# Performance work log

Hardware: AMD Instinct MI355X
Metric: run time of the kernel (lower is better)

## Reference

```python
import jax, jax.numpy as jnp
import numpy as np

HIDDEN = 4096   # hidden_dim
RANK = 16       # lora_rank
ALPHA = 32.0    # lora_alpha
BATCH = 4
SEQ = 4096
TWO_OVER_PI = 2.0 / np.pi


def setup_inputs() -> dict:
    key = jax.random.key(0)
    kx, ka, kb, ksa, ksb = jax.random.split(key, 5)
    x = jax.random.normal(kx, (BATCH, SEQ, HIDDEN), dtype=jnp.float32)
    # int8 pi/2 coefficients (stored as int8, symmetric range)
    A_int8 = jax.random.randint(ka, (HIDDEN, RANK), -127, 128, dtype=jnp.int32).astype(jnp.int8)
    B_int8 = jax.random.randint(kb, (RANK, HIDDEN), -127, 128, dtype=jnp.int32).astype(jnp.int8)
    # per-column (output-channel) dequant scales, small positive values
    scale_A = jax.random.uniform(ksa, (RANK,), jnp.float32, 1e-3, 1e-2)
    scale_B = jax.random.uniform(ksb, (HIDDEN,), jnp.float32, 1e-3, 1e-2)
    return {"x": x, "A_int8": A_int8, "B_int8": B_int8,
            "scale_A": scale_A, "scale_B": scale_B}


def reference(x, A_int8, B_int8, scale_A, scale_B):
    # Dequantize: per-column scale (scale has shape [cols])
    A = A_int8.astype(jnp.float32) * scale_A[None, :]   # [H, R]
    B = B_int8.astype(jnp.float32) * scale_B[None, :]   # [R, H]
    # Low-rank path: x @ A @ B  (rank-16 bottleneck kept explicit)
    h = jnp.einsum('bsh,hr->bsr', x, A)                 # [B, S, R]
    h = jnp.einsum('bsr,rh->bsh', h, B)                 # [B, S, H]
    # y = x + (alpha/r) * sin(h * 2/pi)
    return x + (ALPHA / RANK) * jnp.sin(h * TWO_OVER_PI)
```

## Files before the change

kernel.cpp:

```cpp
#include <hip/hip_runtime.h>

#define H       4096
#define RANK    16
#define NROWS   16384
#define RPB     2
#define TPB     256
#define TWO_OVER_PI 0.63661977236758134f

typedef float f32x4 __attribute__((ext_vector_type(4)));

__global__ __launch_bounds__(256) void pack_ab(const int* __restrict__ A32,
                                               const int* __restrict__ B32,
                                               unsigned int* __restrict__ A8,
                                               unsigned int* __restrict__ B8) {
    int i = blockIdx.x * 256 + threadIdx.x;
    int4 a = ((const int4*)A32)[i];
    A8[i] = ((unsigned)((a.x + 128) & 0xff))       | ((unsigned)((a.y + 128) & 0xff) << 8) |
            ((unsigned)((a.z + 128) & 0xff) << 16) | ((unsigned)((a.w + 128) & 0xff) << 24);

    int c = i & 3, tt = (i >> 2) & 255, r = i >> 10;
    int4 b = ((const int4*)B32)[r * 1024 + c * 256 + tt];
    B8[i] = ((unsigned)((b.x + 128) & 0xff))       | ((unsigned)((b.y + 128) & 0xff) << 8) |
            ((unsigned)((b.z + 128) & 0xff) << 16) | ((unsigned)((b.w + 128) & 0xff) << 24);
}

__global__ __launch_bounds__(TPB, 4) void pilora_fused(
    const float* __restrict__ x,
    const unsigned int* __restrict__ A8,
    const unsigned int* __restrict__ B8,
    const float* __restrict__ sA,
    const float* __restrict__ sB,
    float* __restrict__ out)
{
    const int t    = threadIdx.x;
    const int lane = t & 63;
    const int wid  = t >> 6;
    const int row0 = blockIdx.x * RPB;

    __shared__ __attribute__((aligned(16))) float xs[RPB * H];
    __shared__ float wsum[4][32];
    __shared__ __attribute__((aligned(16))) float hsh[32];
    __shared__ float HsLds[RPB];

    const float* xrow = x + (size_t)row0 * H;
    #pragma unroll
    for (int i = 0; i < 8; ++i) {
        __builtin_amdgcn_global_load_lds(
            (const __attribute__((address_space(1))) unsigned int*)(xrow + i * 1024 + t * 4),
            (__attribute__((address_space(3)))       unsigned int*)(xs   + i * 1024 + t * 4),
            16, 0, 0);
    }
    __syncthreads();

    float w[32];
    #pragma unroll
    for (int j = 0; j < 32; ++j) w[j] = 0.0f;
    float sx0 = 0.0f, sx1 = 0.0f;

    const int4* A16 = (const int4*)A8;
    #pragma unroll
    for (int c = 0; c < 4; ++c) {
        f32x4 xv0 = *(const f32x4*)&xs[      c * 1024 + t * 4];
        f32x4 xv1 = *(const f32x4*)&xs[H +   c * 1024 + t * 4];
        #pragma unroll
        for (int e = 0; e < 4; ++e) {
            int4 q = A16[c * 1024 + t * 4 + e];
            float x0 = xv0[e], x1 = xv1[e];
            sx0 += x0; sx1 += x1;
            int qw[4] = {q.x, q.y, q.z, q.w};
            #pragma unroll
            for (int wi = 0; wi < 4; ++wi) {
                unsigned uw = (unsigned)qw[wi];
                #pragma unroll
                for (int b = 0; b < 4; ++b) {
                    float u = (float)((uw >> (8 * b)) & 0xffu);
                    w[     wi * 4 + b] += x0 * u;
                    w[16 + wi * 4 + b] += x1 * u;
                }
            }
        }
    }
    #pragma unroll
    for (int j = 0; j < 16; ++j) { w[j] -= 128.0f * sx0; w[16 + j] -= 128.0f * sx1; }

    #pragma unroll
    for (int b = 0; b < 5; ++b) {
        int q = (lane >> b) & 1;
        #pragma unroll
        for (int k = 0; k < (16 >> b); ++k) {
            float keep  = q ? w[2 * k + 1] : w[2 * k];
            float send  = q ? w[2 * k]     : w[2 * k + 1];
            float other = __shfl_xor(send, 1 << b, 64);
            w[k] = keep + other;
        }
    }
    w[0] += __shfl_xor(w[0], 32, 64);

    if (lane < 32) wsum[wid][lane] = w[0];
    __syncthreads();

    if (t < 32) {
        float v = wsum[0][t] + wsum[1][t] + wsum[2][t] + wsum[3][t];
        int r = t & 15, rr = t >> 4;
        float hv = v * sA[r];
        hsh[r * 2 + rr] = hv;
        float hs = hv;
        hs += __shfl_xor(hs, 1, 64);
        hs += __shfl_xor(hs, 2, 64);
        hs += __shfl_xor(hs, 4, 64);
        hs += __shfl_xor(hs, 8, 64);
        if (r == 0) HsLds[rr] = 128.0f * hs;
    }
    __syncthreads();

    float hf[32];
    #pragma unroll
    for (int k = 0; k < 8; ++k) *(f32x4*)&hf[k * 4] = *(const f32x4*)&hsh[k * 4];
    float hs0 = HsLds[0], hs1 = HsLds[1];

    float g0[16], g1[16];
    #pragma unroll
    for (int j = 0; j < 16; ++j) { g0[j] = -hs0; g1[j] = -hs1; }

    const int4* Bp = (const int4*)B8;
    #pragma unroll
    for (int r = 0; r < RANK; ++r) {
        float h0 = hf[r * 2 + 0], h1 = hf[r * 2 + 1];
        int4 bw = Bp[r * 256 + t];
        int bwa[4] = {bw.x, bw.y, bw.z, bw.w};
        #pragma unroll
        for (int wi = 0; wi < 4; ++wi) {
            unsigned uw = (unsigned)bwa[wi];
            #pragma unroll
            for (int b = 0; b < 4; ++b) {
                float u = (float)((uw >> (8 * b)) & 0xffu);
                g0[wi * 4 + b] += h0 * u;
                g1[wi * 4 + b] += h1 * u;
            }
        }
    }

    const float4* sB4 = (const float4*)sB;
    f32x4* o4 = (f32x4*)out;
    #pragma unroll
    for (int c = 0; c < 4; ++c) {
        float4 sb = sB4[c * 256 + t];
        float k0 = sb.x * TWO_OVER_PI;
        float k1 = sb.y * TWO_OVER_PI;
        float k2 = sb.z * TWO_OVER_PI;
        float k3 = sb.w * TWO_OVER_PI;
        f32x4 xv0 = *(const f32x4*)&xs[    c * 1024 + t * 4];
        f32x4 xv1 = *(const f32x4*)&xs[H + c * 1024 + t * 4];
        f32x4 o0, o1;
        o0[0] = xv0[0] + 2.0f * __sinf(g0[c * 4 + 0] * k0);
        o0[1] = xv0[1] + 2.0f * __sinf(g0[c * 4 + 1] * k1);
        o0[2] = xv0[2] + 2.0f * __sinf(g0[c * 4 + 2] * k2);
        o0[3] = xv0[3] + 2.0f * __sinf(g0[c * 4 + 3] * k3);
        o1[0] = xv1[0] + 2.0f * __sinf(g1[c * 4 + 0] * k0);
        o1[1] = xv1[1] + 2.0f * __sinf(g1[c * 4 + 1] * k1);
        o1[2] = xv1[2] + 2.0f * __sinf(g1[c * 4 + 2] * k2);
        o1[3] = xv1[3] + 2.0f * __sinf(g1[c * 4 + 3] * k3);
        __builtin_nontemporal_store(o0, &o4[(size_t)(row0 + 0) * 1024 + c * 256 + t]);
        __builtin_nontemporal_store(o1, &o4[(size_t)(row0 + 1) * 1024 + c * 256 + t]);
    }
}

extern "C" void kernel_launch(void* const* d_in, const int* in_sizes, int n_in,
                              void* d_out, int out_size, void* d_ws, size_t ws_size,
                              hipStream_t stream) {
    const float* x   = (const float*)d_in[0];
    const int*   A32 = (const int*)d_in[1];
    const int*   B32 = (const int*)d_in[2];
    const float* sA  = (const float*)d_in[3];
    const float* sB  = (const float*)d_in[4];
    float*       out = (float*)d_out;

    unsigned int* A8 = (unsigned int*)d_ws;
    unsigned int* B8 = A8 + (H * RANK / 4);

    pack_ab<<<(H * RANK / 4) / 256, 256, 0, stream>>>(A32, B32, A8, B8);
    pilora_fused<<<NROWS / RPB, TPB, 0, stream>>>(
        x, A8, B8, sA, sB, out);
}
```

Measured before the change: 465.8 us.

## Process four rows per block with packed FMA and drop LDS staging of x

Each block now handles four rows instead of two, so each int8 weight unpack serves four rows. Accumulation uses 2-wide float vectors so the compiler can emit packed FMA. The LDS staging of x through global_load_lds is removed: x is read straight from global memory in the reduction phase and read a second time in the output phase, counting on cache hits. The risks are a second read of x that may miss the caches and higher register pressure from 64 accumulators per thread.

```diff
diff --git a/kernel.cpp b/kernel.cpp
--- a/kernel.cpp
+++ b/kernel.cpp
@@ -3,11 +3,12 @@
 #define H       4096
 #define RANK    16
 #define NROWS   16384
-#define RPB     2
+#define RPB     4
 #define TPB     256
 #define TWO_OVER_PI 0.63661977236758134f
 
 typedef float f32x4 __attribute__((ext_vector_type(4)));
+typedef float f32x2 __attribute__((ext_vector_type(2)));
 
 __global__ __launch_bounds__(256) void pack_ab(const int* __restrict__ A32,
                                                const int* __restrict__ B32,
@@ -37,36 +38,30 @@
     const int wid  = t >> 6;
     const int row0 = blockIdx.x * RPB;
 
-    __shared__ __attribute__((aligned(16))) float xs[RPB * H];
-    __shared__ float wsum[4][32];
-    __shared__ __attribute__((aligned(16))) float hsh[32];
+    __shared__ float wsum[4][64];
+    __shared__ __attribute__((aligned(16))) float hsh[64];
     __shared__ float HsLds[RPB];
 
-    const float* xrow = x + (size_t)row0 * H;
+    const f32x4* x4 = (const f32x4*)x;
+
+    f32x2 w01[16], w23[16];
     #pragma unroll
-    for (int i = 0; i < 8; ++i) {
-        __builtin_amdgcn_global_load_lds(
-            (const __attribute__((address_space(1))) unsigned int*)(xrow + i * 1024 + t * 4),
-            (__attribute__((address_space(3)))       unsigned int*)(xs   + i * 1024 + t * 4),
-            16, 0, 0);
-    }
-    __syncthreads();
-
-    float w[32];
-    #pragma unroll
-    for (int j = 0; j < 32; ++j) w[j] = 0.0f;
-    float sx0 = 0.0f, sx1 = 0.0f;
+    for (int j = 0; j < 16; ++j) { w01[j] = (f32x2)0.0f; w23[j] = (f32x2)0.0f; }
+    f32x2 sx01 = (f32x2)0.0f, sx23 = (f32x2)0.0f;
 
     const int4* A16 = (const int4*)A8;
     #pragma unroll
     for (int c = 0; c < 4; ++c) {
-        f32x4 xv0 = *(const f32x4*)&xs[      c * 1024 + t * 4];
-        f32x4 xv1 = *(const f32x4*)&xs[H +   c * 1024 + t * 4];
+        f32x4 xv0 = x4[(row0 + 0) * 1024 + c * 256 + t];
+        f32x4 xv1 = x4[(row0 + 1) * 1024 + c * 256 + t];
+        f32x4 xv2 = x4[(row0 + 2) * 1024 + c * 256 + t];
+        f32x4 xv3 = x4[(row0 + 3) * 1024 + c * 256 + t];
         #pragma unroll
         for (int e = 0; e < 4; ++e) {
             int4 q = A16[c * 1024 + t * 4 + e];
-            float x0 = xv0[e], x1 = xv1[e];
-            sx0 += x0; sx1 += x1;
+            f32x2 x01; x01[0] = xv0[e]; x01[1] = xv1[e];
+            f32x2 x23; x23[0] = xv2[e]; x23[1] = xv3[e];
+            sx01 += x01; sx23 += x23;
             int qw[4] = {q.x, q.y, q.z, q.w};
             #pragma unroll
             for (int wi = 0; wi < 4; ++wi) {
@@ -74,36 +69,46 @@
                 #pragma unroll
                 for (int b = 0; b < 4; ++b) {
                     float u = (float)((uw >> (8 * b)) & 0xffu);
-                    w[     wi * 4 + b] += x0 * u;
-                    w[16 + wi * 4 + b] += x1 * u;
+                    f32x2 u2; u2[0] = u; u2[1] = u;
+                    w01[wi * 4 + b] += x01 * u2;
+                    w23[wi * 4 + b] += x23 * u2;
                 }
             }
         }
     }
     #pragma unroll
-    for (int j = 0; j < 16; ++j) { w[j] -= 128.0f * sx0; w[16 + j] -= 128.0f * sx1; }
+    for (int j = 0; j < 16; ++j) {
+        w01[j] -= sx01 * 128.0f;
+        w23[j] -= sx23 * 128.0f;
+    }
+
+    float wf[64];
+    #pragma unroll
+    for (int r = 0; r < 16; ++r) {
+        wf[ 0 + r] = w01[r][0];
+        wf[16 + r] = w01[r][1];
+        wf[32 + r] = w23[r][0];
+        wf[48 + r] = w23[r][1];
+    }
 
     #pragma unroll
-    for (int b = 0; b < 5; ++b) {
+    for (int b = 0; b < 6; ++b) {
         int q = (lane >> b) & 1;
         #pragma unroll
-        for (int k = 0; k < (16 >> b); ++k) {
-            float keep  = q ? w[2 * k + 1] : w[2 * k];
-            float send  = q ? w[2 * k]     : w[2 * k + 1];
-            float other = __shfl_xor(send, 1 << b, 64);
-            w[k] = keep + other;
+        for (int k = 0; k < (32 >> b); ++k) {
+            float keep = q ? wf[2 * k + 1] : wf[2 * k];
+            float send = q ? wf[2 * k]     : wf[2 * k + 1];
+            wf[k] = keep + __shfl_xor(send, 1 << b, 64);
         }
     }
-    w[0] += __shfl_xor(w[0], 32, 64);
-
-    if (lane < 32) wsum[wid][lane] = w[0];
+    wsum[wid][lane] = wf[0];
     __syncthreads();
 
-    if (t < 32) {
+    if (t < 64) {
         float v = wsum[0][t] + wsum[1][t] + wsum[2][t] + wsum[3][t];
         int r = t & 15, rr = t >> 4;
         float hv = v * sA[r];
-        hsh[r * 2 + rr] = hv;
+        hsh[r * 4 + rr] = hv;
         float hs = hv;
         hs += __shfl_xor(hs, 1, 64);
         hs += __shfl_xor(hs, 2, 64);
@@ -113,19 +118,20 @@
     }
     __syncthreads();
 
-    float hf[32];
+    f32x2 nh01, nh23;
+    nh01[0] = -HsLds[0]; nh01[1] = -HsLds[1];
+    nh23[0] = -HsLds[2]; nh23[1] = -HsLds[3];
+
+    f32x2 g01[16], g23[16];
     #pragma unroll
-    for (int k = 0; k < 8; ++k) *(f32x4*)&hf[k * 4] = *(const f32x4*)&hsh[k * 4];
-    float hs0 = HsLds[0], hs1 = HsLds[1];
-
-    float g0[16], g1[16];
-    #pragma unroll
-    for (int j = 0; j < 16; ++j) { g0[j] = -hs0; g1[j] = -hs1; }
+    for (int j = 0; j < 16; ++j) { g01[j] = nh01; g23[j] = nh23; }
 
     const int4* Bp = (const int4*)B8;
-    #pragma unroll
+    #pragma unroll 4
     for (int r = 0; r < RANK; ++r) {
-        float h0 = hf[r * 2 + 0], h1 = hf[r * 2 + 1];
+        f32x4 hr = *(const f32x4*)&hsh[r * 4];
+        f32x2 h01; h01[0] = hr[0]; h01[1] = hr[1];
+        f32x2 h23; h23[0] = hr[2]; h23[1] = hr[3];
         int4 bw = Bp[r * 256 + t];
         int bwa[4] = {bw.x, bw.y, bw.z, bw.w};
         #pragma unroll
@@ -134,34 +140,35 @@
             #pragma unroll
             for (int b = 0; b < 4; ++b) {
                 float u = (float)((uw >> (8 * b)) & 0xffu);
-                g0[wi * 4 + b] += h0 * u;
-                g1[wi * 4 + b] += h1 * u;
+                f32x2 u2; u2[0] = u; u2[1] = u;
+                g01[wi * 4 + b] += h01 * u2;
+                g23[wi * 4 + b] += h23 * u2;
             }
         }
     }
 
-    const float4* sB4 = (const float4*)sB;
+    const f32x4* sB4 = (const f32x4*)sB;
     f32x4* o4 = (f32x4*)out;
     #pragma unroll
     for (int c = 0; c < 4; ++c) {
-        float4 sb = sB4[c * 256 + t];
-        float k0 = sb.x * TWO_OVER_PI;
-        float k1 = sb.y * TWO_OVER_PI;
-        float k2 = sb.z * TWO_OVER_PI;
-        float k3 = sb.w * TWO_OVER_PI;
-        f32x4 xv0 = *(const f32x4*)&xs[    c * 1024 + t * 4];
-        f32x4 xv1 = *(const f32x4*)&xs[H + c * 1024 + t * 4];
-        f32x4 o0, o1;
-        o0[0] = xv0[0] + 2.0f * __sinf(g0[c * 4 + 0] * k0);
-        o0[1] = xv0[1] + 2.0f * __sinf(g0[c * 4 + 1] * k1);
-        o0[2] = xv0[2] + 2.0f * __sinf(g0[c * 4 + 2] * k2);
-        o0[3] = xv0[3] + 2.0f * __sinf(g0[c * 4 + 3] * k3);
-        o1[0] = xv1[0] + 2.0f * __sinf(g1[c * 4 + 0] * k0);
-        o1[1] = xv1[1] + 2.0f * __sinf(g1[c * 4 + 1] * k1);
-        o1[2] = xv1[2] + 2.0f * __sinf(g1[c * 4 + 2] * k2);
-        o1[3] = xv1[3] + 2.0f * __sinf(g1[c * 4 + 3] * k3);
-        __builtin_nontemporal_store(o0, &o4[(size_t)(row0 + 0) * 1024 + c * 256 + t]);
-        __builtin_nontemporal_store(o1, &o4[(size_t)(row0 + 1) * 1024 + c * 256 + t]);
+        f32x4 sb  = sB4[c * 256 + t];
+        f32x4 xv0 = x4[(row0 + 0) * 1024 + c * 256 + t];
+        f32x4 xv1 = x4[(row0 + 1) * 1024 + c * 256 + t];
+        f32x4 xv2 = x4[(row0 + 2) * 1024 + c * 256 + t];
+        f32x4 xv3 = x4[(row0 + 3) * 1024 + c * 256 + t];
+        f32x4 o0, o1, o2, o3;
+        #pragma unroll
+        for (int b = 0; b < 4; ++b) {
+            float k = sb[b] * TWO_OVER_PI;
+            o0[b] = xv0[b] + 2.0f * __sinf(g01[c * 4 + b][0] * k);
+            o1[b] = xv1[b] + 2.0f * __sinf(g01[c * 4 + b][1] * k);
+            o2[b] = xv2[b] + 2.0f * __sinf(g23[c * 4 + b][0] * k);
+            o3[b] = xv3[b] + 2.0f * __sinf(g23[c * 4 + b][1] * k);
+        }
+        __builtin_nontemporal_store(o0, &o4[(row0 + 0) * 1024 + c * 256 + t]);
+        __builtin_nontemporal_store(o1, &o4[(row0 + 1) * 1024 + c * 256 + t]);
+        __builtin_nontemporal_store(o2, &o4[(row0 + 2) * 1024 + c * 256 + t]);
+        __builtin_nontemporal_store(o3, &o4[(row0 + 3) * 1024 + c * 256 + t]);
     }
 }
 
```

New measurement: 1.126 ms. +141.7%, slower.
